# Kernel optimization log

Measured on AMD Instinct MI355X. Metric: run time of the kernel, lower is better.

Reference implementation:

```python
import jax, jax.numpy as jnp
import numpy as np

R = 3                 # corr_radius
STRIDE = 4
RES = (384, 512)      # model_resolution (H, W)
G = 2 * R + 1         # 7: support grid side


def setup_inputs() -> dict:
    key = jax.random.key(0)
    ks = jax.random.split(key, 16)
    B, S, N, C = 1, 8, 1024, 128
    H0, W0 = RES[0] // STRIDE, RES[1] // STRIDE  # 96, 128
    inp = {}
    for i in range(4):
        h, w = H0 >> i, W0 >> i
        inp[f"fmaps{i}"] = jax.random.normal(ks[i], (B, S, C, h, w), jnp.float32)
        inp[f"track{i}"] = jax.random.normal(ks[4 + i], (B, G * G, N, C), jnp.float32)
    inp["coords"] = jax.random.uniform(ks[8], (B, S, N, 2), jnp.float32) * jnp.asarray([W0 - 1.0, H0 - 1.0], jnp.float32)
    inp["vis"] = jax.random.normal(ks[9], (B, S, N, 1), jnp.float32)
    inp["conf"] = jax.random.normal(ks[10], (B, S, N, 1), jnp.float32)
    r2 = G * G
    inp["w1"] = jax.random.normal(ks[11], (r2 * r2, 384), jnp.float32) * (1.0 / np.sqrt(r2 * r2))
    inp["b1"] = jnp.zeros((384,), jnp.float32)
    inp["w2"] = jax.random.normal(ks[12], (384, 256), jnp.float32) * (1.0 / np.sqrt(384))
    inp["b2"] = jnp.zeros((256,), jnp.float32)
    inp["time_emb"] = jax.random.normal(ks[13], (1, S, 1110), jnp.float32) * 0.02
    return inp


def bilinear_sample(fmap, x, y):
    """fmap: (BT, C, H, W); x, y: (BT, M) pixel coords. Border padding, align_corners=True
    (matches torch grid_sample as used by co-tracker's bilinear_sampler)."""
    BT, C, H, W = fmap.shape
    x0f = jnp.floor(x)
    y0f = jnp.floor(y)
    wx = (x - x0f)[:, None, :]
    wy = (y - y0f)[:, None, :]
    x0 = jnp.clip(x0f.astype(jnp.int32), 0, W - 1)
    x1 = jnp.clip(x0f.astype(jnp.int32) + 1, 0, W - 1)
    y0 = jnp.clip(y0f.astype(jnp.int32), 0, H - 1)
    y1 = jnp.clip(y0f.astype(jnp.int32) + 1, 0, H - 1)
    flat = fmap.reshape(BT, C, H * W)

    def g(yi, xi):
        idx = (yi * W + xi)[:, None, :]  # (BT, 1, M)
        return jnp.take_along_axis(flat, idx, axis=2)  # (BT, C, M)

    return (g(y0, x0) * (1 - wx) * (1 - wy) + g(y0, x1) * wx * (1 - wy)
            + g(y1, x0) * (1 - wx) * wy + g(y1, x1) * wx * wy)


def posenc(x, min_deg=0, max_deg=10):
    scales = jnp.asarray([2.0 ** i for i in range(min_deg, max_deg)], x.dtype)
    xb = (x[..., None, :] * scales[:, None]).reshape(x.shape[:-1] + (-1,))
    four = jnp.sin(jnp.concatenate([xb, xb + 0.5 * jnp.pi], axis=-1))
    return jnp.concatenate([x, four], axis=-1)


def reference(fmaps0, fmaps1, fmaps2, fmaps3, track0, track1, track2, track3,
              coords, vis, conf, w1, b1, w2, b2, time_emb):
    B, S, N, _ = coords.shape
    fps = [fmaps0, fmaps1, fmaps2, fmaps3]
    tps = [track0, track1, track2, track3]
    d = jnp.linspace(-R, R, G)
    xoff, yoff = jnp.meshgrid(d, d, indexing='ij')  # (7,7): rows = x offset, cols = y offset

    embs = []
    for lvl in range(4):
        fm = fps[lvl]
        C, H, W = fm.shape[2], fm.shape[3], fm.shape[4]
        c = coords.reshape(B * S, N, 1, 1, 2) / (2.0 ** lvl)
        x = c[..., 0] + xoff          # (B*S, N, 7, 7)
        y = c[..., 1] + yoff
        M = N * G * G
        sampled = bilinear_sample(fm.reshape(B * S, C, H, W), x.reshape(B * S, M), y.reshape(B * S, M))
        corr_feat = sampled.reshape(B, S, C, N, G, G).transpose(0, 1, 3, 4, 5, 2)  # (B,S,N,7,7,C)
        track = tps[lvl].reshape(B, G, G, N, C).transpose(0, 3, 1, 2, 4)           # (B,N,7,7,C)
        vol = jnp.einsum('btnhwc,bnijc->btnhwij', corr_feat, track)                # (B,S,N,7,7,7,7)
        h = jax.nn.gelu(vol.reshape(B * S * N, G * G * G * G) @ w1 + b1, approximate=False)
        embs.append(h @ w2 + b2)
    corr_embs = jnp.concatenate(embs, axis=-1).reshape(B, S, N, -1)  # (B,S,N,1024)

    rel_f = jnp.pad(coords[:, :-1] - coords[:, 1:], ((0, 0), (0, 1), (0, 0), (0, 0)))
    rel_b = jnp.pad(coords[:, 1:] - coords[:, :-1], ((0, 0), (1, 0), (0, 0), (0, 0)))
    scale = jnp.asarray([RES[1], RES[0]], jnp.float32) / STRIDE
    rel_emb = posenc(jnp.concatenate([rel_f / scale, rel_b / scale], axis=-1))  # (B,S,N,84)

    x = jnp.concatenate([vis, conf, corr_embs, rel_emb], axis=-1)  # (B,S,N,1110)
    x = x.transpose(0, 2, 1, 3).reshape(B * N, S, -1) + time_emb
    return x.reshape(B, N, S, -1)
```

## Files before the change

kernel.cpp:

```cpp
#include <hip/hip_runtime.h>
#include <math.h>


#define SN 8
#define NN 1024
#define CC 128
#define K1P 2432
#define H1 384
#define H2 256
#define DOUT 1110

typedef short bf16x8 __attribute__((ext_vector_type(8)));
typedef float f32x4 __attribute__((ext_vector_type(4)));

__device__ inline unsigned short f2b(float x) {
    union { float f; unsigned u; } v; v.f = x;
    unsigned r = v.u + 0x7FFFu + ((v.u >> 16) & 1u);
    return (unsigned short)(r >> 16);
}
__device__ inline float b2f(unsigned short u) {
    union { unsigned u; float f; } v; v.u = (unsigned)u << 16; return v.f;
}
__device__ inline void gll16(const void* g, void* l) {
    __builtin_amdgcn_global_load_lds(
        (const __attribute__((address_space(1))) void*)g,
        (__attribute__((address_space(3))) void*)l, 16, 0, 0);
}
__device__ inline int swz(int row, int g) {
    return row * 128 + ((g ^ (row & 7)) << 3);
}

__global__ __launch_bounds__(256) void conv_fmap_kernel(
    const float* __restrict__ in, unsigned short* __restrict__ outp,
    int H, int W)
{
    const int Hp = H + 8, Wp = W + 8;
    const int s = blockIdx.x / Hp, yp = blockIdx.x % Hp;
    const int y = min(max(yp - 4, 0), H - 1);
    const float* src = in + (size_t)s * CC * H * W + (size_t)y * W;
    unsigned short* dst = outp + ((size_t)s * Hp + yp) * Wp * CC;
    for (int idx = threadIdx.x; idx < Wp * CC; idx += 256) {
        int xp = idx >> 7, c = idx & 127;
        int x = min(max(xp - 4, 0), W - 1);
        dst[idx] = f2b(src[(size_t)c * H * W + x]);
    }
}

__global__ __launch_bounds__(256, 3) void sample_vol_kernel(
    const unsigned short* __restrict__ fq0, const unsigned short* __restrict__ fq1,
    const unsigned short* __restrict__ fq2, const unsigned short* __restrict__ fq3,
    const float* __restrict__ tk0, const float* __restrict__ tk1,
    const float* __restrict__ tk2, const float* __restrict__ tk3,
    const float* __restrict__ coords,
    unsigned short* __restrict__ vol,
    int lv0)
{
    __shared__ __align__(16) unsigned short patch[80 * 128];
    __shared__ __align__(16) unsigned short trk[64 * 128];
    __shared__ __align__(16) unsigned short pcL[80 * 66];
    const int n = blockIdx.x & 1023, g = blockIdx.x >> 10;
    const int lvl = lv0 + g;
    const unsigned short* fpad = (lvl == 0) ? fq0 : (lvl == 1) ? fq1
                               : (lvl == 2) ? fq2 : fq3;
    const float* track = (lvl == 0) ? tk0 : (lvl == 1) ? tk1
                       : (lvl == 2) ? tk2 : tk3;
    const int Wp = (128 >> lvl) + 8;
    const int t = threadIdx.x;
    const int lane = t & 63, wv = t >> 6;
    const int rsub = lane & 15, kq = lane >> 4;
    const float inv = 1.0f / (float)(1 << lvl);
    const size_t plane = (size_t)((96 >> lvl) + 8) * Wp * CC;

    int poff[5], ldso[5];
    #pragma unroll
    for (int i = 0; i < 5; ++i) {
        int task64 = wv * 5 + i;
        int point = task64 * 4 + (lane >> 4);
        int v = point / 10, xs = point - v * 10;
        int j = (lane & 15) ^ (point & 7);
        poff[i] = (v * Wp + xs) * CC + j * 8;
        ldso[i] = task64 * 512;
    }

    float cxa[SN], cya[SN];
    #pragma unroll
    for (int s = 0; s < SN; ++s) {
        float2 c2 = *(const float2*)&coords[((size_t)s * NN + n) * 2];
        cxa[s] = c2.x * inv; cya[s] = c2.y * inv;
    }

    unsigned lutA[5], lutB[5];
    #pragma unroll
    for (int i = 0; i < 5; ++i) {
        int d = t + i * 256;
        int o0 = 2 * d, o1 = 2 * d + 1;
        lutA[i] = 0xFFFFFFFFu; lutB[i] = 0xFFFFFFFFu;
        if (o0 < 2401) {
            int ab = o0 / 49, ij = o0 - 49 * ab, a = ab / 7, b = ab - 7 * a;
            lutA[i] = (unsigned)((b * 10 + a) * 66 + ij);
        }
        if (o1 < 2401) {
            int ab = o1 / 49, ij = o1 - 49 * ab, a = ab / 7, b = ab - 7 * a;
            lutB[i] = (unsigned)((b * 10 + a) * 66 + ij);
        }
    }

    int fx = (int)floorf(cxa[0]), fy = (int)floorf(cya[0]);
    int e = (fx - 3) & ~1;
    {
        const unsigned short* base = fpad + ((fy + 1) * Wp + (e + 4)) * CC;
        #pragma unroll
        for (int i = 0; i < 5; ++i) gll16(base + poff[i], &patch[ldso[i]]);
    }
    for (int task = t; task < 49 * 16; task += 256) {
        int row = task >> 4, gg = task & 15;
        const float* srcp = &track[((size_t)row * NN + n) * CC + gg * 8];
        float4 f0 = *(const float4*)srcp;
        float4 f1 = *(const float4*)(srcp + 4);
        bf16x8 v8;
        v8[0] = f2b(f0.x); v8[1] = f2b(f0.y); v8[2] = f2b(f0.z); v8[3] = f2b(f0.w);
        v8[4] = f2b(f1.x); v8[5] = f2b(f1.y); v8[6] = f2b(f1.z); v8[7] = f2b(f1.w);
        *(bf16x8*)&trk[swz(row, gg)] = v8;
    }

    #pragma unroll
    for (int sl = 0; sl < SN; ++sl) {
        const float wx = cxa[sl] - (float)fx, wy = cya[sl] - (float)fy;
        const float w00 = (1.f - wx) * (1.f - wy), w10 = wx * (1.f - wy);
        const float w01 = (1.f - wx) * wy,         w11 = wx * wy;
        const int offs = (fx - 3 - e) * 66;

        asm volatile("s_waitcnt vmcnt(0)" ::: "memory");
        __syncthreads();

        {
            f32x4 acc[5] = {};
            #pragma unroll
            for (int kk = 0; kk < 4; ++kk) {
                int gg = kk * 4 + kq;
                bf16x8 b = *(const bf16x8*)&trk[swz(wv * 16 + rsub, gg)];
                #pragma unroll
                for (int ti = 0; ti < 5; ++ti) {
                    bf16x8 a = *(const bf16x8*)&patch[swz(ti * 16 + rsub, gg)];
                    acc[ti] = __builtin_amdgcn_mfma_f32_16x16x32_bf16(a, b, acc[ti], 0, 0, 0);
                }
            }
            const int col = wv * 16 + rsub;
            #pragma unroll
            for (int ti = 0; ti < 5; ++ti)
                #pragma unroll
                for (int r = 0; r < 4; ++r)
                    pcL[(ti * 16 + kq * 4 + r) * 66 + col] = f2b(acc[ti][r]);
        }
        __syncthreads();

        if (sl + 1 < SN) {
            fx = (int)floorf(cxa[sl + 1]); fy = (int)floorf(cya[sl + 1]);
            e = (fx - 3) & ~1;
            const unsigned short* base =
                fpad + (size_t)(sl + 1) * plane + ((fy + 1) * Wp + (e + 4)) * CC;
            #pragma unroll
            for (int i = 0; i < 5; ++i) gll16(base + poff[i], &patch[ldso[i]]);
        }

        {
            unsigned* vrow32 = (unsigned*)(vol + ((size_t)(g * SN + sl) * NN + n) * K1P);
            #pragma unroll
            for (int i = 0; i < 5; ++i) {
                int d = t + i * 256;
                if (d < K1P / 2) {
                    unsigned lo = 0, hi = 0;
                    if (lutA[i] != 0xFFFFFFFFu) {
                        int idx = (int)lutA[i] + offs;
                        float v = w00 * b2f(pcL[idx])       + w10 * b2f(pcL[idx + 66])
                                + w01 * b2f(pcL[idx + 660]) + w11 * b2f(pcL[idx + 726]);
                        lo = f2b(v);
                    }
                    if (lutB[i] != 0xFFFFFFFFu) {
                        int idx = (int)lutB[i] + offs;
                        float v = w00 * b2f(pcL[idx])       + w10 * b2f(pcL[idx + 66])
                                + w01 * b2f(pcL[idx + 660]) + w11 * b2f(pcL[idx + 726]);
                        hi = f2b(v);
                    }
                    vrow32[d] = lo | (hi << 16);
                }
            }
        }
    }
}

__global__ __launch_bounds__(256, 3) void gemm1_kernel(
    const unsigned short* __restrict__ A,
    const unsigned short* __restrict__ Bt,
    const float* __restrict__ bias,
    unsigned short* __restrict__ Hout)
{
    __shared__ __align__(16) unsigned short As[3 * 128 * 32];
    __shared__ __align__(16) unsigned short Bs[3 * 128 * 32];
    const int h = blockIdx.x, q = gridDim.x >> 3;
    const int l = (h & 7) * q + (h >> 3);
    const int m0 = (l / 3) * 128, n0 = (l % 3) * 128;
    const int t = threadIdx.x, lane = t & 63, wv = t >> 6;
    const int wm = wv >> 1, wn = wv & 1;
    const int rsub = lane & 15, kq = lane >> 4;

    const int rA0 = t >> 2, sA0 = (t & 3) ^ ((rA0 >> 1) & 3);
    const int rA1 = (t + 256) >> 2, sA1 = ((t + 256) & 3) ^ ((rA1 >> 1) & 3);
    const unsigned short* gA0 = A  + (size_t)(m0 + rA0) * K1P + sA0 * 8;
    const unsigned short* gA1 = A  + (size_t)(m0 + rA1) * K1P + sA1 * 8;
    const unsigned short* gB0 = Bt + (size_t)(n0 + rA0) * K1P + sA0 * 8;
    const unsigned short* gB1 = Bt + (size_t)(n0 + rA1) * K1P + sA1 * 8;
    const int chunk0 = (t & ~63) * 8, chunk1 = (256 + (t & ~63)) * 8;

    f32x4 acc[4][4] = {};

    const int NSTEP = K1P / 32;
    #pragma unroll
    for (int p = 0; p < 3; ++p) {
        size_t ko = (size_t)p * 32;
        int lb = p * 4096;
        gll16(gA0 + ko, &As[lb + chunk0]); gll16(gA1 + ko, &As[lb + chunk1]);
        gll16(gB0 + ko, &Bs[lb + chunk0]); gll16(gB1 + ko, &Bs[lb + chunk1]);
    }
    int cur = 0;
    for (int st = 0; st < NSTEP; ++st) {
        const int rem = NSTEP - 1 - st;
        if (rem >= 2)      asm volatile("s_waitcnt vmcnt(8)" ::: "memory");
        else if (rem == 1) asm volatile("s_waitcnt vmcnt(4)" ::: "memory");
        else               asm volatile("s_waitcnt vmcnt(0)" ::: "memory");
        __builtin_amdgcn_s_barrier();
        __builtin_amdgcn_sched_barrier(0);
        const int lb = cur * 4096;
        bf16x8 af[4], bfr[4];
        #pragma unroll
        for (int mi = 0; mi < 4; ++mi) {
            int r = wm * 64 + mi * 16 + rsub;
            int phys = r * 4 + (kq ^ ((r >> 1) & 3));
            af[mi] = *(const bf16x8*)&As[lb + phys * 8];
        }
        #pragma unroll
        for (int ni = 0; ni < 4; ++ni) {
            int r = wn * 64 + ni * 16 + rsub;
            int phys = r * 4 + (kq ^ ((r >> 1) & 3));
            bfr[ni] = *(const bf16x8*)&Bs[lb + phys * 8];
        }
        #pragma unroll
        for (int mi = 0; mi < 4; ++mi)
            #pragma unroll
            for (int ni = 0; ni < 4; ++ni)
                acc[mi][ni] = __builtin_amdgcn_mfma_f32_16x16x32_bf16(
                    af[mi], bfr[ni], acc[mi][ni], 0, 0, 0);
        __builtin_amdgcn_sched_barrier(0);
        __builtin_amdgcn_s_barrier();
        __builtin_amdgcn_sched_barrier(0);
        if (st + 3 < NSTEP) {
            size_t ko = (size_t)(st + 3) * 32;
            gll16(gA0 + ko, &As[lb + chunk0]);
            gll16(gA1 + ko, &As[lb + chunk1]);
            gll16(gB0 + ko, &Bs[lb + chunk0]);
            gll16(gB1 + ko, &Bs[lb + chunk1]);
        }
        cur = (cur == 2) ? 0 : cur + 1;
    }
    #pragma unroll
    for (int mi = 0; mi < 4; ++mi) {
        int row = m0 + wm * 64 + mi * 16 + kq * 4;
        #pragma unroll
        for (int ni = 0; ni < 4; ++ni) {
            int col = n0 + wn * 64 + ni * 16 + rsub;
            float bcol = bias[col];
            #pragma unroll
            for (int r = 0; r < 4; ++r) {
                float x = acc[mi][ni][r] + bcol;
                float gg = 0.5f * x * (1.f + erff(x * 0.70710678118654752f));
                Hout[(size_t)(row + r) * H1 + col] = f2b(gg);
            }
        }
    }
}

__global__ __launch_bounds__(256, 3) void gemm2_kernel(
    const unsigned short* __restrict__ A,
    const unsigned short* __restrict__ Bt,
    const float* __restrict__ bias,
    const float* __restrict__ te,
    float* __restrict__ out,
    int lv0)
{
    __shared__ __align__(16) unsigned short As[3 * 128 * 32];
    __shared__ __align__(16) unsigned short Bs[3 * 128 * 32];
    const int h = blockIdx.x, q = gridDim.x >> 3;
    const int l = (h & 7) * q + (h >> 3);
    const int m0 = (l >> 1) * 128, n0 = (l & 1) * 128;
    const int t = threadIdx.x, lane = t & 63, wv = t >> 6;
    const int wm = wv >> 1, wn = wv & 1;
    const int rsub = lane & 15, kq = lane >> 4;

    const int rA0 = t >> 2, sA0 = (t & 3) ^ ((rA0 >> 1) & 3);
    const int rA1 = (t + 256) >> 2, sA1 = ((t + 256) & 3) ^ ((rA1 >> 1) & 3);
    const unsigned short* gA0 = A  + (size_t)(m0 + rA0) * H1 + sA0 * 8;
    const unsigned short* gA1 = A  + (size_t)(m0 + rA1) * H1 + sA1 * 8;
    const unsigned short* gB0 = Bt + (size_t)(n0 + rA0) * H1 + sA0 * 8;
    const unsigned short* gB1 = Bt + (size_t)(n0 + rA1) * H1 + sA1 * 8;
    const int chunk0 = (t & ~63) * 8, chunk1 = (256 + (t & ~63)) * 8;

    f32x4 acc[4][4] = {};

    const int NSTEP = H1 / 32;
    #pragma unroll
    for (int p = 0; p < 3; ++p) {
        size_t ko = (size_t)p * 32;
        int lb = p * 4096;
        gll16(gA0 + ko, &As[lb + chunk0]); gll16(gA1 + ko, &As[lb + chunk1]);
        gll16(gB0 + ko, &Bs[lb + chunk0]); gll16(gB1 + ko, &Bs[lb + chunk1]);
    }
    int cur = 0;
    for (int st = 0; st < NSTEP; ++st) {
        const int rem = NSTEP - 1 - st;
        if (rem >= 2)      asm volatile("s_waitcnt vmcnt(8)" ::: "memory");
        else if (rem == 1) asm volatile("s_waitcnt vmcnt(4)" ::: "memory");
        else               asm volatile("s_waitcnt vmcnt(0)" ::: "memory");
        __builtin_amdgcn_s_barrier();
        __builtin_amdgcn_sched_barrier(0);
        const int lb = cur * 4096;
        bf16x8 af[4], bfr[4];
        #pragma unroll
        for (int mi = 0; mi < 4; ++mi) {
            int r = wm * 64 + mi * 16 + rsub;
            int phys = r * 4 + (kq ^ ((r >> 1) & 3));
            af[mi] = *(const bf16x8*)&As[lb + phys * 8];
        }
        #pragma unroll
        for (int ni = 0; ni < 4; ++ni) {
            int r = wn * 64 + ni * 16 + rsub;
            int phys = r * 4 + (kq ^ ((r >> 1) & 3));
            bfr[ni] = *(const bf16x8*)&Bs[lb + phys * 8];
        }
        #pragma unroll
        for (int mi = 0; mi < 4; ++mi)
            #pragma unroll
            for (int ni = 0; ni < 4; ++ni)
                acc[mi][ni] = __builtin_amdgcn_mfma_f32_16x16x32_bf16(
                    af[mi], bfr[ni], acc[mi][ni], 0, 0, 0);
        __builtin_amdgcn_sched_barrier(0);
        __builtin_amdgcn_s_barrier();
        __builtin_amdgcn_sched_barrier(0);
        if (st + 3 < NSTEP) {
            size_t ko = (size_t)(st + 3) * 32;
            gll16(gA0 + ko, &As[lb + chunk0]);
            gll16(gA1 + ko, &As[lb + chunk1]);
            gll16(gB0 + ko, &Bs[lb + chunk0]);
            gll16(gB1 + ko, &Bs[lb + chunk1]);
        }
        cur = (cur == 2) ? 0 : cur + 1;
    }
    #pragma unroll
    for (int mi = 0; mi < 4; ++mi) {
        int rowb = m0 + wm * 64 + mi * 16 + kq * 4;
        #pragma unroll
        for (int ni = 0; ni < 4; ++ni) {
            int col = n0 + wn * 64 + ni * 16 + rsub;
            float bcol = bias[col];
            #pragma unroll
            for (int r = 0; r < 4; ++r) {
                int row = rowb + r;
                int g = row >> 13, s = (row >> 10) & 7, n = row & 1023;
                int dcol = 2 + (lv0 + g) * H2 + col;
                out[((size_t)n * SN + s) * DOUT + dcol] =
                    acc[mi][ni][r] + bcol + te[s * DOUT + dcol];
            }
        }
    }
}

__global__ __launch_bounds__(256) void conv_t_kernel(
    const float* __restrict__ in, unsigned short* __restrict__ outp,
    int K, int Nw, int Kp)
{
    __shared__ float tile[32][33];
    const int kb = blockIdx.x * 32, nb = blockIdx.y * 32;
    const int tx = threadIdx.x & 31, ty = threadIdx.x >> 5;
    #pragma unroll
    for (int i = 0; i < 32; i += 8) {
        int k = kb + ty + i, nn = nb + tx;
        tile[ty + i][tx] = (k < K && nn < Nw) ? in[(size_t)k * Nw + nn] : 0.f;
    }
    __syncthreads();
    #pragma unroll
    for (int i = 0; i < 32; i += 8) {
        int nn = nb + ty + i, k = kb + tx;
        if (nn < Nw) outp[(size_t)nn * Kp + k] = f2b(tile[tx][ty + i]);
    }
}

__global__ __launch_bounds__(128) void tail_kernel(
    const float* __restrict__ coords, const float* __restrict__ vis,
    const float* __restrict__ conf, const float* __restrict__ te,
    float* __restrict__ out)
{
    const int b = blockIdx.x;
    const int n = b >> 3, s = b & 7;
    const int d = threadIdx.x;
    if (d >= 86) return;
    const size_t ob = (size_t)b * DOUT;
    if (d == 0) {
        out[ob + 0] = vis[(size_t)s * NN + n] + te[s * DOUT + 0];
    } else if (d == 1) {
        out[ob + 1] = conf[(size_t)s * NN + n] + te[s * DOUT + 1];
    } else {
        int rd = d - 2;
        float cx = coords[((size_t)s * NN + n) * 2 + 0];
        float cy = coords[((size_t)s * NN + n) * 2 + 1];
        float rfx = 0.f, rfy = 0.f, rbx = 0.f, rby = 0.f;
        if (s < SN - 1) {
            rfx = cx - coords[((size_t)(s + 1) * NN + n) * 2 + 0];
            rfy = cy - coords[((size_t)(s + 1) * NN + n) * 2 + 1];
        }
        if (s > 0) {
            rbx = cx - coords[((size_t)(s - 1) * NN + n) * 2 + 0];
            rby = cy - coords[((size_t)(s - 1) * NN + n) * 2 + 1];
        }
        float r4[4] = {rfx / 128.f, rfy / 96.f, rbx / 128.f, rby / 96.f};
        float val;
        if (rd < 4) {
            val = r4[rd];
        } else if (rd < 44) {
            int q = rd - 4; int deg = q >> 2, comp = q & 3;
            val = sinf(r4[comp] * (float)(1 << deg));
        } else {
            int q = rd - 44; int deg = q >> 2, comp = q & 3;
            val = sinf(r4[comp] * (float)(1 << deg) + 1.57079632679489662f);
        }
        int od = 1026 + rd;
        out[ob + od] = val + te[s * DOUT + od];
    }
}

extern "C" void kernel_launch(void* const* d_in, const int* in_sizes, int n_in,
                              void* d_out, int out_size, void* d_ws, size_t ws_size,
                              hipStream_t stream) {
    const float* fmaps[4] = {(const float*)d_in[0], (const float*)d_in[2],
                             (const float*)d_in[4], (const float*)d_in[6]};
    const float* track[4] = {(const float*)d_in[1], (const float*)d_in[3],
                             (const float*)d_in[5], (const float*)d_in[7]};
    const float* coords = (const float*)d_in[8];
    const float* vis    = (const float*)d_in[9];
    const float* conf   = (const float*)d_in[10];
    const float* w1     = (const float*)d_in[11];
    const float* b1     = (const float*)d_in[12];
    const float* w2     = (const float*)d_in[13];
    const float* b2     = (const float*)d_in[14];
    const float* te     = (const float*)d_in[15];
    float* out = (float*)d_out;

    const int Hs[4] = {96, 48, 24, 12};
    const int Ws[4] = {128, 64, 32, 16};

    char* wsb = (char*)d_ws;
    unsigned short* w1t = (unsigned short*)wsb;
    size_t off = (size_t)H1 * K1P * 2;
    unsigned short* w2t = (unsigned short*)(wsb + off);
    off += (size_t)H2 * H1 * 2;
    unsigned short* fpad[4];
    for (int l = 0; l < 4; ++l) {
        fpad[l] = (unsigned short*)(wsb + off);
        off += (size_t)SN * (Hs[l] + 8) * (Ws[l] + 8) * CC * 2;
    }
    off += 512;
    const size_t fixed = off;
    int n_lv = 4;
    while (n_lv > 1 &&
           fixed + (size_t)n_lv * SN * NN * (K1P + H1) * 2 > ws_size)
        n_lv >>= 1;
    unsigned short* volb = (unsigned short*)(wsb + fixed);
    unsigned short* hb   = volb + (size_t)n_lv * SN * NN * K1P;

    conv_t_kernel<<<dim3(K1P / 32, H1 / 32), 256, 0, stream>>>(w1, w1t, 2401, H1, K1P);
    conv_t_kernel<<<dim3(H1 / 32, H2 / 32), 256, 0, stream>>>(w2, w2t, H1, H2, H1);
    for (int l = 0; l < 4; ++l)
        conv_fmap_kernel<<<SN * (Hs[l] + 8), 256, 0, stream>>>(
            fmaps[l], fpad[l], Hs[l], Ws[l]);

    for (int lv0 = 0; lv0 < 4; lv0 += n_lv) {
        sample_vol_kernel<<<n_lv * NN, 256, 0, stream>>>(
            fpad[0], fpad[1], fpad[2], fpad[3],
            track[0], track[1], track[2], track[3],
            coords, volb, lv0);
        const int rows = n_lv * SN * NN;
        gemm1_kernel<<<(rows / 128) * 3, 256, 0, stream>>>(volb, w1t, b1, hb);
        gemm2_kernel<<<(rows / 128) * 2, 256, 0, stream>>>(hb, w2t, b2, te, out, lv0);
    }
    tail_kernel<<<SN * NN, 128, 0, stream>>>(coords, vis, conf, te, out);
}
```

Baseline: 347.5 us.

## Compute bilinear interpolation of correlation patch as MFMA with sparse weight matrix

The scalar bilinear gather over the LDS correlation patch is replaced by a second MFMA. Each block builds a 49x100 bf16 weight matrix holding the four bilinear weights per output position and multiplies it by the transposed patch correlations. The first MFMA operands are swapped so the patch is stored transposed. The kernel also replaces __syncthreads with explicit barriers and partial vmcnt waits so the next patch prefetch overlaps, and drops the occupancy hint from 3 to 2 because of the added LDS. The weights are now rounded to bf16, and stores go out per element instead of as packed 32-bit words.

```diff
diff --git a/kernel.cpp b/kernel.cpp
--- a/kernel.cpp
+++ b/kernel.cpp
@@ -17,9 +17,6 @@
     union { float f; unsigned u; } v; v.f = x;
     unsigned r = v.u + 0x7FFFu + ((v.u >> 16) & 1u);
     return (unsigned short)(r >> 16);
-}
-__device__ inline float b2f(unsigned short u) {
-    union { unsigned u; float f; } v; v.u = (unsigned)u << 16; return v.f;
 }
 __device__ inline void gll16(const void* g, void* l) {
     __builtin_amdgcn_global_load_lds(
@@ -46,7 +43,7 @@
     }
 }
 
-__global__ __launch_bounds__(256, 3) void sample_vol_kernel(
+__global__ __launch_bounds__(256, 2) void sample_vol_kernel(
     const unsigned short* __restrict__ fq0, const unsigned short* __restrict__ fq1,
     const unsigned short* __restrict__ fq2, const unsigned short* __restrict__ fq3,
     const float* __restrict__ tk0, const float* __restrict__ tk1,
@@ -57,7 +54,8 @@
 {
     __shared__ __align__(16) unsigned short patch[80 * 128];
     __shared__ __align__(16) unsigned short trk[64 * 128];
-    __shared__ __align__(16) unsigned short pcL[80 * 66];
+    __shared__ __align__(16) unsigned short pcT[64 * 104];
+    __shared__ __align__(16) unsigned short Wl[64 * 104];
     const int n = blockIdx.x & 1023, g = blockIdx.x >> 10;
     const int lvl = lv0 + g;
     const unsigned short* fpad = (lvl == 0) ? fq0 : (lvl == 1) ? fq1
@@ -89,21 +87,8 @@
         cxa[s] = c2.x * inv; cya[s] = c2.y * inv;
     }
 
-    unsigned lutA[5], lutB[5];
-    #pragma unroll
-    for (int i = 0; i < 5; ++i) {
-        int d = t + i * 256;
-        int o0 = 2 * d, o1 = 2 * d + 1;
-        lutA[i] = 0xFFFFFFFFu; lutB[i] = 0xFFFFFFFFu;
-        if (o0 < 2401) {
-            int ab = o0 / 49, ij = o0 - 49 * ab, a = ab / 7, b = ab - 7 * a;
-            lutA[i] = (unsigned)((b * 10 + a) * 66 + ij);
-        }
-        if (o1 < 2401) {
-            int ab = o1 / 49, ij = o1 - 49 * ab, a = ab / 7, b = ab - 7 * a;
-            lutB[i] = (unsigned)((b * 10 + a) * 66 + ij);
-        }
-    }
+    const int wa = t / 7, wb = t - 7 * (t / 7);
+    int obase = wb * 10 + wa;
 
     int fx = (int)floorf(cxa[0]), fy = (int)floorf(cya[0]);
     int e = (fx - 3) & ~1;
@@ -122,37 +107,61 @@
         v8[4] = f2b(f1.x); v8[5] = f2b(f1.y); v8[6] = f2b(f1.z); v8[7] = f2b(f1.w);
         *(bf16x8*)&trk[swz(row, gg)] = v8;
     }
+    {
+        unsigned* T32 = (unsigned*)trk;
+        for (int i = t; i < 15 * 64; i += 256) T32[49 * 64 + i] = 0;
+        unsigned* W32 = (unsigned*)Wl;
+        for (int i = t; i < 49 * 52; i += 256) W32[i] = 0;
+        unsigned* P32 = (unsigned*)pcT;
+        for (int i = t; i < 64 * 12; i += 256) {
+            int r = i / 12, c = i - 12 * r;
+            P32[r * 52 + 40 + c] = 0;
+        }
+    }
 
     #pragma unroll
     for (int sl = 0; sl < SN; ++sl) {
         const float wx = cxa[sl] - (float)fx, wy = cya[sl] - (float)fy;
         const float w00 = (1.f - wx) * (1.f - wy), w10 = wx * (1.f - wy);
         const float w01 = (1.f - wx) * wy,         w11 = wx * wy;
-        const int offs = (fx - 3 - e) * 66;
-
-        asm volatile("s_waitcnt vmcnt(0)" ::: "memory");
-        __syncthreads();
+        const int off = fx - 3 - e;
+
+        if (sl == 0) asm volatile("s_waitcnt vmcnt(0) lgkmcnt(0)" ::: "memory");
+        else         asm volatile("s_waitcnt vmcnt(16) lgkmcnt(0)" ::: "memory");
+        __builtin_amdgcn_sched_barrier(0);
+        __builtin_amdgcn_s_barrier();
+        __builtin_amdgcn_sched_barrier(0);
 
         {
             f32x4 acc[5] = {};
             #pragma unroll
             for (int kk = 0; kk < 4; ++kk) {
                 int gg = kk * 4 + kq;
-                bf16x8 b = *(const bf16x8*)&trk[swz(wv * 16 + rsub, gg)];
+                bf16x8 a = *(const bf16x8*)&trk[swz(wv * 16 + rsub, gg)];
                 #pragma unroll
                 for (int ti = 0; ti < 5; ++ti) {
-                    bf16x8 a = *(const bf16x8*)&patch[swz(ti * 16 + rsub, gg)];
+                    bf16x8 b = *(const bf16x8*)&patch[swz(ti * 16 + rsub, gg)];
                     acc[ti] = __builtin_amdgcn_mfma_f32_16x16x32_bf16(a, b, acc[ti], 0, 0, 0);
                 }
             }
-            const int col = wv * 16 + rsub;
             #pragma unroll
             for (int ti = 0; ti < 5; ++ti)
                 #pragma unroll
                 for (int r = 0; r < 4; ++r)
-                    pcL[(ti * 16 + kq * 4 + r) * 66 + col] = f2b(acc[ti][r]);
-        }
-        __syncthreads();
+                    pcT[(wv * 16 + kq * 4 + r) * 104 + ti * 16 + rsub] = f2b(acc[ti][r]);
+        }
+        if (t < 49) {
+            int base = wb * 10 + off + wa;
+            unsigned short* wr = &Wl[t * 104];
+            wr[obase] = 0; wr[obase + 1] = 0; wr[obase + 10] = 0; wr[obase + 11] = 0;
+            wr[base] = f2b(w00); wr[base + 1] = f2b(w10);
+            wr[base + 10] = f2b(w01); wr[base + 11] = f2b(w11);
+            obase = base;
+        }
+
+        asm volatile("s_waitcnt lgkmcnt(0)" ::: "memory");
+        __builtin_amdgcn_s_barrier();
+        __builtin_amdgcn_sched_barrier(0);
 
         if (sl + 1 < SN) {
             fx = (int)floorf(cxa[sl + 1]); fy = (int)floorf(cya[sl + 1]);
@@ -162,27 +171,32 @@
             #pragma unroll
             for (int i = 0; i < 5; ++i) gll16(base + poff[i], &patch[ldso[i]]);
         }
+        __builtin_amdgcn_sched_barrier(0);
 
         {
-            unsigned* vrow32 = (unsigned*)(vol + ((size_t)(g * SN + sl) * NN + n) * K1P);
-            #pragma unroll
-            for (int i = 0; i < 5; ++i) {
-                int d = t + i * 256;
-                if (d < K1P / 2) {
-                    unsigned lo = 0, hi = 0;
-                    if (lutA[i] != 0xFFFFFFFFu) {
-                        int idx = (int)lutA[i] + offs;
-                        float v = w00 * b2f(pcL[idx])       + w10 * b2f(pcL[idx + 66])
-                                + w01 * b2f(pcL[idx + 660]) + w11 * b2f(pcL[idx + 726]);
-                        lo = f2b(v);
-                    }
-                    if (lutB[i] != 0xFFFFFFFFu) {
-                        int idx = (int)lutB[i] + offs;
-                        float v = w00 * b2f(pcL[idx])       + w10 * b2f(pcL[idx + 66])
-                                + w01 * b2f(pcL[idx + 660]) + w11 * b2f(pcL[idx + 726]);
-                        hi = f2b(v);
-                    }
-                    vrow32[d] = lo | (hi << 16);
+            f32x4 acc2[4] = {};
+            #pragma unroll
+            for (int kk = 0; kk < 3; ++kk) {
+                int g2 = (kk * 4 + kq) * 8;
+                bf16x8 a = *(const bf16x8*)&Wl[(wv * 16 + rsub) * 104 + g2];
+                #pragma unroll
+                for (int ni = 0; ni < 4; ++ni) {
+                    bf16x8 b = *(const bf16x8*)&pcT[(ni * 16 + rsub) * 104 + g2];
+                    acc2[ni] = __builtin_amdgcn_mfma_f32_16x16x32_bf16(a, b, acc2[ni], 0, 0, 0);
+                }
+            }
+            unsigned short* vrow = vol + ((size_t)(g * SN + sl) * NN + n) * K1P;
+            #pragma unroll
+            for (int ni = 0; ni < 4; ++ni) {
+                int ij = ni * 16 + rsub;
+                #pragma unroll
+                for (int r = 0; r < 4; ++r) {
+                    int ab = wv * 16 + kq * 4 + r;
+                    bool valid = (ab < 49) && (ij < 49);
+                    int addr = valid ? (ab * 49 + ij)
+                                     : (2401 + (lane + (ni * 4 + r) * 7) % 31);
+                    unsigned short val = valid ? f2b(acc2[ni][r]) : (unsigned short)0;
+                    vrow[addr] = val;
                 }
             }
         }
```

Result: slower. 397.1 us (+14.3%).
